# Performance work log

Measured on AMD Instinct MI355X. Metric: run time of the kernel, lower is better.

## Reference

```python
import jax, jax.numpy as jnp
import numpy as np

PS = 8   # patch_size
W2 = 2   # micro_patch_window_size

def _dct_basis(N=PS):
    # Orthonormal DCT-II basis: D[k, n] = s(k) * cos(pi*(2n+1)*k/(2N))
    n = np.arange(N)
    D = np.cos(np.pi * (2 * n[None, :] + 1) * n[:, None] / (2 * N))
    scale = np.full(N, np.sqrt(2.0 / N))
    scale[0] = np.sqrt(1.0 / N)
    return jnp.asarray((D * scale[:, None]).astype(np.float32))


def setup_inputs() -> dict:
    key = jax.random.key(0)
    x = jax.random.normal(key, (64, 3, 512, 512), dtype=jnp.float32)
    return {"x": x}


def reference(x):
    B, C, H, W = x.shape
    PH, PW = H // PS, W // PS
    D = _dct_basis().astype(x.dtype)
    # patches: (B, PH, PW, C, PS, PS)
    patches = x.reshape(B, C, PH, PS, PW, PS).transpose(0, 2, 4, 1, 3, 5)
    # 2D orthonormal DCT-II on the last two dims: D @ X @ D^T as one einsum
    d = jnp.einsum('bpqcij,ki,lj->bpqckl', patches, D, D)
    # Faithful to the torch boolean-mask + view: masked-select flattens in
    # (B, PH, PW, C, w, w) order, then is *reinterpreted* as (B, C, PH, PW, w, w)
    low = d[..., :W2, :W2].reshape(B, C, PH, PW, W2, W2)
    low = low.transpose(0, 2, 3, 1, 4, 5)
    high = d[..., PS - W2:, PS - W2:].reshape(B, C, PH, PW, W2, W2)
    high = high[..., ::-1, ::-1]          # flip(4).flip(5)
    high = high.transpose(0, 2, 3, 1, 4, 5)
    return low, high
```

## Files before the change

### kernel.cpp

```cpp
#include <hip/hip_runtime.h>


__global__ __launch_bounds__(192) void freq_dct_kernel(
    const float* __restrict__ x, float* __restrict__ out_low, float* __restrict__ out_high)
{
    const float DR[4][8] = {
        { 0.35355339059327373f, 0.35355339059327373f, 0.35355339059327373f, 0.35355339059327373f,
          0.35355339059327373f, 0.35355339059327373f, 0.35355339059327373f, 0.35355339059327373f },
        { 0.49039264020161522f, 0.41573480615127262f, 0.27778511650980109f, 0.09754516100806412f,
         -0.09754516100806412f,-0.27778511650980109f,-0.41573480615127262f,-0.49039264020161522f },
        { 0.19134171618254489f,-0.46193976625564337f, 0.46193976625564337f,-0.19134171618254489f,
         -0.19134171618254489f, 0.46193976625564337f,-0.46193976625564337f, 0.19134171618254489f },
        { 0.09754516100806412f,-0.27778511650980109f, 0.41573480615127262f,-0.49039264020161522f,
          0.49039264020161522f,-0.41573480615127262f, 0.27778511650980109f,-0.09754516100806412f }
    };

    __shared__ float lds_lo[768];
    __shared__ float lds_hi[768];

    const int bss = blockIdx.x;
    const int b   = bss >> 6;
    const int ss  = bss & 63;
    const int idx = threadIdx.x;
    const int rr  = idx >> 6;
    const int tt  = idx & 63;

    const int m   = rr * 4096 + ss * 64 + tt;
    const int p   = m / 192;
    const int rem = m - p * 192;
    const int q   = rem / 3;
    const int c   = rem - q * 3;

    const float* src = x + ((size_t)(b * 3 + c) * 512 + (size_t)p * 8) * 512 + (size_t)q * 8;

    float t[4][8];
    #pragma unroll
    for (int k = 0; k < 4; ++k)
        #pragma unroll
        for (int j = 0; j < 8; ++j) t[k][j] = 0.0f;

    #pragma unroll
    for (int i = 0; i < 8; ++i) {
        const float4 a0 = *reinterpret_cast<const float4*>(src + (size_t)i * 512);
        const float4 a1 = *reinterpret_cast<const float4*>(src + (size_t)i * 512 + 4);
        const float row[8] = { a0.x, a0.y, a0.z, a0.w, a1.x, a1.y, a1.z, a1.w };
        #pragma unroll
        for (int k = 0; k < 4; ++k) {
            const float dk = DR[k][i];
            #pragma unroll
            for (int j = 0; j < 8; ++j) t[k][j] = fmaf(dk, row[j], t[k][j]);
        }
    }

    float lv[4], hv[4];
    #pragma unroll
    for (int a = 0; a < 2; ++a) {
        #pragma unroll
        for (int l = 0; l < 2; ++l) {
            float accL = 0.0f, accH = 0.0f;
            #pragma unroll
            for (int j = 0; j < 8; ++j) {
                accL = fmaf(t[a][j],     DR[l][j],     accL);
                accH = fmaf(t[3 - a][j], DR[3 - l][j], accH);
            }
            lv[a * 2 + l] = accL;
            hv[a * 2 + l] = accH;
        }
    }

    const int base = tt * 12 + rr * 4;
    *reinterpret_cast<float4*>(&lds_lo[base]) = make_float4(lv[0], lv[1], lv[2], lv[3]);
    *reinterpret_cast<float4*>(&lds_hi[base]) = make_float4(hv[0], hv[1], hv[2], hv[3]);
    __syncthreads();

    const size_t off = (size_t)bss * 768 + (size_t)idx * 4;
    const float4 lo4 = reinterpret_cast<const float4*>(lds_lo)[idx];
    const float4 hi4 = reinterpret_cast<const float4*>(lds_hi)[idx];
    *reinterpret_cast<float4*>(out_low  + off) = lo4;
    *reinterpret_cast<float4*>(out_high + off) = hi4;
}

extern "C" void kernel_launch(void* const* d_in, const int* in_sizes, int n_in,
                              void* d_out, int out_size, void* d_ws, size_t ws_size,
                              hipStream_t stream) {
    const float* x = (const float*)d_in[0];
    float* out  = (float*)d_out;
    float* low  = out;
    float* high = out + 3145728;

    hipLaunchKernelGGL(freq_dct_kernel, dim3(4096), dim3(192), 0, stream,
                       x, low, high);
}
```

Before: 43.32 us.

## Reorder DCT to column-first per row, add nontemporal stores and occupancy hint

```diff
diff --git a/kernel.cpp b/kernel.cpp
--- a/kernel.cpp
+++ b/kernel.cpp
@@ -1,7 +1,9 @@
 #include <hip/hip_runtime.h>
 
 
-__global__ __launch_bounds__(192) void freq_dct_kernel(
+typedef float floatx4 __attribute__((ext_vector_type(4)));
+
+__global__ __launch_bounds__(192, 6) void freq_dct_kernel(
     const float* __restrict__ x, float* __restrict__ out_low, float* __restrict__ out_high)
 {
     const float DR[4][8] = {
@@ -33,38 +35,30 @@
 
     const float* src = x + ((size_t)(b * 3 + c) * 512 + (size_t)p * 8) * 512 + (size_t)q * 8;
 
-    float t[4][8];
-    #pragma unroll
-    for (int k = 0; k < 4; ++k)
-        #pragma unroll
-        for (int j = 0; j < 8; ++j) t[k][j] = 0.0f;
+    float lv[4] = {0.f, 0.f, 0.f, 0.f};
+    float hv[4] = {0.f, 0.f, 0.f, 0.f};
 
     #pragma unroll
     for (int i = 0; i < 8; ++i) {
         const float4 a0 = *reinterpret_cast<const float4*>(src + (size_t)i * 512);
         const float4 a1 = *reinterpret_cast<const float4*>(src + (size_t)i * 512 + 4);
         const float row[8] = { a0.x, a0.y, a0.z, a0.w, a1.x, a1.y, a1.z, a1.w };
+
+        float u[4] = {0.f, 0.f, 0.f, 0.f};
         #pragma unroll
-        for (int k = 0; k < 4; ++k) {
-            const float dk = DR[k][i];
+        for (int j = 0; j < 8; ++j) {
             #pragma unroll
-            for (int j = 0; j < 8; ++j) t[k][j] = fmaf(dk, row[j], t[k][j]);
+            for (int l = 0; l < 4; ++l) u[l] = fmaf(row[j], DR[l][j], u[l]);
         }
-    }
-
-    float lv[4], hv[4];
-    #pragma unroll
-    for (int a = 0; a < 2; ++a) {
         #pragma unroll
-        for (int l = 0; l < 2; ++l) {
-            float accL = 0.0f, accH = 0.0f;
+        for (int a = 0; a < 2; ++a) {
+            const float dl = DR[a][i];
+            const float dh = DR[3 - a][i];
             #pragma unroll
-            for (int j = 0; j < 8; ++j) {
-                accL = fmaf(t[a][j],     DR[l][j],     accL);
-                accH = fmaf(t[3 - a][j], DR[3 - l][j], accH);
+            for (int l = 0; l < 2; ++l) {
+                lv[a * 2 + l] = fmaf(dl, u[l],     lv[a * 2 + l]);
+                hv[a * 2 + l] = fmaf(dh, u[3 - l], hv[a * 2 + l]);
             }
-            lv[a * 2 + l] = accL;
-            hv[a * 2 + l] = accH;
         }
     }
 
@@ -74,10 +68,10 @@
     __syncthreads();
 
     const size_t off = (size_t)bss * 768 + (size_t)idx * 4;
-    const float4 lo4 = reinterpret_cast<const float4*>(lds_lo)[idx];
-    const float4 hi4 = reinterpret_cast<const float4*>(lds_hi)[idx];
-    *reinterpret_cast<float4*>(out_low  + off) = lo4;
-    *reinterpret_cast<float4*>(out_high + off) = hi4;
+    const floatx4 lo4 = *reinterpret_cast<const floatx4*>(&lds_lo[idx * 4]);
+    const floatx4 hi4 = *reinterpret_cast<const floatx4*>(&lds_hi[idx * 4]);
+    __builtin_nontemporal_store(lo4, reinterpret_cast<floatx4*>(out_low  + off));
+    __builtin_nontemporal_store(hi4, reinterpret_cast<floatx4*>(out_high + off));
 }
 
 extern "C" void kernel_launch(void* const* d_in, const int* in_sizes, int n_in,
```

Measured after the change: 57.56 us. +32.9%, slower.
